# Optimization experiments

Measured on AMD Instinct MI355X. Metric: run time of the kernel, lower is better.

## Reference

```python
import jax, jax.numpy as jnp
import numpy as np

B, D, C = 8192, 1024, 4096  # batch, d_model, num_clusters (all active)
EPS = 1e-12  # matches F.normalize eps


def _l2_normalize(x):
    n = jnp.linalg.norm(x, axis=-1, keepdims=True)
    return x / jnp.maximum(n, EPS)


def setup_inputs() -> dict:
    key = jax.random.key(0)
    k1, k2 = jax.random.split(key)
    embedding = jax.random.normal(k1, (B, D), dtype=jnp.float32)
    centroids = jax.random.normal(k2, (C, D), dtype=jnp.float32)  # buffer, all active
    return {"embedding": embedding, "centroids": centroids}


def reference(embedding, centroids):
    # Fused equivalent of the per-centroid Python loop:
    # cosine sim of normalized embedding vs each normalized centroid.
    emb_n = _l2_normalize(embedding)        # [B, D]
    cen_n = _l2_normalize(centroids)        # [C, D]
    sims = jnp.clip(emb_n @ cen_n.T, 0.0, 1.0)  # [B, C], per-sim clamp to [0,1]
    max_sim = jnp.max(sims, axis=-1)        # [B]
    closest = jnp.argmax(sims, axis=-1)     # [B] int
    novelty = jnp.clip(jnp.sqrt(1.0 - max_sim), 0.0, 1.0)  # [B]
    return novelty, closest
```

## Files before the change

### kernel.cpp

```cpp
#include <hip/hip_runtime.h>
#include <math.h>

#define B_ROWS 8192
#define C_COLS 4096
#define D_DIM  1024
#define EPSN   1e-12f

typedef float v4f __attribute__((ext_vector_type(4)));
typedef short v8s __attribute__((ext_vector_type(8)));

__device__ __forceinline__ unsigned short bf16_rtn(float x) {
    unsigned int u = __float_as_uint(x);
    u += 0x7fffu + ((u >> 16) & 1u);
    return (unsigned short)(u >> 16);
}

__device__ __forceinline__ bool better_vi(float v, int i, float V, int I) {
    return (v > V) || (v == V && i < I);
}

__global__ __launch_bounds__(256) void prep_kernel(
    const float* __restrict__ emb, const float* __restrict__ cen,
    unsigned short* __restrict__ Ah, unsigned short* __restrict__ Bh,
    float* __restrict__ inv_a, float* __restrict__ inv_b)
{
    const int lane = threadIdx.x & 63;
    const int wid  = blockIdx.x * 4 + (threadIdx.x >> 6);
    const float* src; unsigned short* dst; float* invp; int r;
    if (wid < B_ROWS) { src = emb; r = wid;          dst = Ah; invp = inv_a; }
    else              { src = cen; r = wid - B_ROWS; dst = Bh; invp = inv_b; }

    const float* rp = src + (size_t)r * D_DIM;
    float4 v[4];
    float ss = 0.0f;
    #pragma unroll
    for (int j = 0; j < 4; ++j) {
        v[j] = *(const float4*)(rp + (j * 64 + lane) * 4);
        ss += v[j].x * v[j].x + v[j].y * v[j].y + v[j].z * v[j].z + v[j].w * v[j].w;
    }
    #pragma unroll
    for (int off = 1; off < 64; off <<= 1) ss += __shfl_xor(ss, off, 64);

    const float iv = 1.0f / fmaxf(sqrtf(ss), EPSN);
    if (lane == 0) invp[r] = iv;

    unsigned short* dp = dst + (size_t)r * D_DIM;
    #pragma unroll
    for (int j = 0; j < 4; ++j) {
        ushort4 H;
        H.x = bf16_rtn(v[j].x * iv);
        H.y = bf16_rtn(v[j].y * iv);
        H.z = bf16_rtn(v[j].z * iv);
        H.w = bf16_rtn(v[j].w * iv);
        *(ushort4*)(dp + (j * 64 + lane) * 4) = H;
    }
}

#define GLD16(gp, lp) \
    __builtin_amdgcn_global_load_lds( \
        (const __attribute__((address_space(1))) void*)(gp), \
        (__attribute__((address_space(3))) void*)(lp), 16, 0, 0)

__global__ __launch_bounds__(512, 4) void simmax_kernel(
    const unsigned short* __restrict__ Ahg, const unsigned short* __restrict__ Bhg,
    float* __restrict__ p1v, int* __restrict__ p1i,
    float* __restrict__ p2v, int* __restrict__ p2i)
{
    __shared__ unsigned short lds[24576];

    const int tid    = threadIdx.x;
    const int L      = tid & 63;
    const int w      = tid >> 6;
    const int lane15 = L & 15;
    const int quad   = L >> 4;
    const int wr     = w >> 1;
    const int wc     = w & 1;

    const int bid = blockIdx.x;
    const int xc  = bid & 7;
    const int s   = bid >> 3;
    const int bx  = xc * 4 + (s & 3);
    const int by  = s >> 2;
    const int row0 = bx * 256;
    const int c0   = by * 128;

    const int scol = (tid & 7) ^ ((tid >> 3) & 7);
    const unsigned short* aB = Ahg + (size_t)(row0 + (tid >> 3)) * D_DIM + scol * 8;
    const unsigned short* bB = Bhg + (size_t)(c0   + (tid >> 3)) * D_DIM + scol * 8;
    const int wofs = w * 512;

#define STAGE_ALL(kb) do { \
    GLD16(aB + (kb),           &lds[0     + wofs]); \
    GLD16(aB + 65536  + (kb),  &lds[4096  + wofs]); \
    GLD16(aB + 131072 + (kb),  &lds[8192  + wofs]); \
    GLD16(aB + 196608 + (kb),  &lds[12288 + wofs]); \
    GLD16(bB + (kb),           &lds[16384 + wofs]); \
    GLD16(bB + 65536  + (kb),  &lds[20480 + wofs]); \
} while (0)

    v4f acc[4][4];
    #pragma unroll
    for (int mt = 0; mt < 4; ++mt)
        #pragma unroll
        for (int nt = 0; nt < 4; ++nt) acc[mt][nt] = (v4f)0.0f;

    int rAo[4], rBo[4];
    #pragma unroll
    for (int t = 0; t < 4; ++t) {
        rAo[t] = (wr * 64 + t * 16 + lane15) * 64;
        rBo[t] = 16384 + (wc * 64 + t * 16 + lane15) * 64;
    }
    const int s7 = lane15 & 7;
    const int cq[2] = { (quad ^ s7) * 8, ((4 + quad) ^ s7) * 8 };

    for (int kc = 0; kc < D_DIM / 64; ++kc) {
        STAGE_ALL(kc * 64);
        __syncthreads();

        #pragma unroll
        for (int h = 0; h < 2; ++h) {
            v8s fah[4], fbh[4];
            #pragma unroll
            for (int t = 0; t < 4; ++t) {
                fah[t] = *(const v8s*)&lds[rAo[t] + cq[h]];
                fbh[t] = *(const v8s*)&lds[rBo[t] + cq[h]];
            }
            #pragma unroll
            for (int mt = 0; mt < 4; ++mt)
                #pragma unroll
                for (int nt = 0; nt < 4; ++nt)
                    acc[mt][nt] = __builtin_amdgcn_mfma_f32_16x16x32_bf16(
                        fah[mt], fbh[nt], acc[mt][nt], 0, 0, 0);
        }
        __syncthreads();
    }

    const int pc = by * 2 + wc;
    #pragma unroll
    for (int mt = 0; mt < 4; ++mt) {
        #pragma unroll
        for (int r = 0; r < 4; ++r) {
            float a1v = acc[mt][0][r];
            int   a1i = c0 + wc * 64 + 0 * 16 + lane15;
            float a2v = -1e30f;
            int   a2i = 0x7fffffff;
            #pragma unroll
            for (int nt = 1; nt < 4; ++nt) {
                float v  = acc[mt][nt][r];
                int   ci = c0 + wc * 64 + nt * 16 + lane15;
                if (better_vi(v, ci, a1v, a1i))      { a2v = a1v; a2i = a1i; a1v = v; a1i = ci; }
                else if (better_vi(v, ci, a2v, a2i)) { a2v = v;   a2i = ci; }
            }
            #pragma unroll
            for (int off = 8; off; off >>= 1) {
                float b1v = __shfl_down(a1v, off, 64); int b1i = __shfl_down(a1i, off, 64);
                float b2v = __shfl_down(a2v, off, 64); int b2i = __shfl_down(a2i, off, 64);
                if (better_vi(b1v, b1i, a1v, a1i)) {
                    if (better_vi(a1v, a1i, b2v, b2i)) { a2v = a1v; a2i = a1i; }
                    else                               { a2v = b2v; a2i = b2i; }
                    a1v = b1v; a1i = b1i;
                } else if (better_vi(b1v, b1i, a2v, a2i)) {
                    a2v = b1v; a2i = b1i;
                }
            }
            if (lane15 == 0) {
                int rg = row0 + wr * 64 + mt * 16 + quad * 4 + r;
                size_t ix = (size_t)rg * 64 + pc;
                p1v[ix] = a1v; p1i[ix] = a1i;
                p2v[ix] = a2v; p2i[ix] = a2i;
            }
        }
    }
}

__global__ __launch_bounds__(256) void finalize_kernel(
    const float* __restrict__ emb, const float* __restrict__ cen,
    const float* __restrict__ inv_a, const float* __restrict__ inv_b,
    const float* __restrict__ p1v, const int* __restrict__ p1i,
    const float* __restrict__ p2v, const int* __restrict__ p2i,
    float* __restrict__ out)
{
    const int lane = threadIdx.x & 63;
    const int row  = blockIdx.x * 4 + (threadIdx.x >> 6);
    const size_t base = (size_t)row * 64 + lane;

    float v[4]; int ix[4];
    v[0] = p1v[base]; ix[0] = p1i[base];
    v[1] = p2v[base]; ix[1] = p2i[base];
    v[2] = -1e30f;    ix[2] = 0x7ffffffe;
    v[3] = -1e30f;    ix[3] = 0x7fffffff;

    #pragma unroll
    for (int off = 1; off < 64; off <<= 1) {
        float ov[4]; int oi[4];
        #pragma unroll
        for (int k = 0; k < 4; ++k) {
            ov[k] = __shfl_xor(v[k],  off, 64);
            oi[k] = __shfl_xor(ix[k], off, 64);
        }
        #pragma unroll
        for (int k = 0; k < 4; ++k) {
            float bv = ov[k]; int bi = oi[k];
            bool b0 = better_vi(bv, bi, v[0], ix[0]);
            bool b1 = better_vi(bv, bi, v[1], ix[1]);
            bool b2 = better_vi(bv, bi, v[2], ix[2]);
            bool b3 = better_vi(bv, bi, v[3], ix[3]);
            float nv3 = b2 ? v[2] : (b3 ? bv : v[3]); int ni3 = b2 ? ix[2] : (b3 ? bi : ix[3]);
            float nv2 = b1 ? v[1] : (b2 ? bv : v[2]); int ni2 = b1 ? ix[1] : (b2 ? bi : ix[2]);
            float nv1 = b0 ? v[0] : (b1 ? bv : v[1]); int ni1 = b0 ? ix[0] : (b1 ? bi : ix[1]);
            float nv0 = b0 ? bv   : v[0];             int ni0 = b0 ? bi    : ix[0];
            v[0] = nv0; ix[0] = ni0; v[1] = nv1; ix[1] = ni1;
            v[2] = nv2; ix[2] = ni2; v[3] = nv3; ix[3] = ni3;
        }
    }

    const float* er = emb + (size_t)row * D_DIM;
    const float* cr0 = cen + (size_t)ix[0] * D_DIM;
    const float* cr1 = cen + (size_t)ix[1] * D_DIM;
    const float* cr2 = cen + (size_t)ix[2] * D_DIM;
    const float* cr3 = cen + (size_t)ix[3] * D_DIM;

    float d[4] = { 0.0f, 0.0f, 0.0f, 0.0f };
    #pragma unroll
    for (int j = 0; j < 4; ++j) {
        int e = (j * 64 + lane) * 4;
        float4 ev = *(const float4*)(er  + e);
        float4 c0 = *(const float4*)(cr0 + e);
        float4 c1 = *(const float4*)(cr1 + e);
        float4 c2 = *(const float4*)(cr2 + e);
        float4 c3 = *(const float4*)(cr3 + e);
        d[0] += ev.x * c0.x + ev.y * c0.y + ev.z * c0.z + ev.w * c0.w;
        d[1] += ev.x * c1.x + ev.y * c1.y + ev.z * c1.z + ev.w * c1.w;
        d[2] += ev.x * c2.x + ev.y * c2.y + ev.z * c2.z + ev.w * c2.w;
        d[3] += ev.x * c3.x + ev.y * c3.y + ev.z * c3.z + ev.w * c3.w;
    }
    #pragma unroll
    for (int off = 1; off < 64; off <<= 1) {
        #pragma unroll
        for (int c = 0; c < 4; ++c) d[c] += __shfl_xor(d[c], off, 64);
    }

    if (lane == 0) {
        const float ia = inv_a[row];
        float m = -1e30f; int ci = 0x7fffffff;
        #pragma unroll
        for (int c = 0; c < 4; ++c) {
            float s = d[c] * ia * inv_b[ix[c]];
            if (better_vi(s, ix[c], m, ci)) { m = s; ci = ix[c]; }
        }
        if (m <= 0.0f) ci = 0;
        float ms = fminf(fmaxf(m, 0.0f), 1.0f);
        out[row]          = fminf(fmaxf(sqrtf(1.0f - ms), 0.0f), 1.0f);
        out[B_ROWS + row] = (float)ci;
    }
}

extern "C" void kernel_launch(void* const* d_in, const int* in_sizes, int n_in,
                              void* d_out, int out_size, void* d_ws, size_t ws_size,
                              hipStream_t stream)
{
    const float* emb = (const float*)d_in[0];
    const float* cen = (const float*)d_in[1];
    float* out = (float*)d_out;

    unsigned short* Ahp = (unsigned short*)d_ws;
    unsigned short* Bhp = Ahp + (size_t)B_ROWS * D_DIM;
    float* inv_a = (float*)(Bhp + (size_t)C_COLS * D_DIM);
    float* inv_b = inv_a + B_ROWS;
    float* p1v   = inv_b + C_COLS;
    int*   p1i   = (int*)(p1v + (size_t)64 * B_ROWS);
    float* p2v   = (float*)(p1i + (size_t)64 * B_ROWS);
    int*   p2i   = (int*)(p2v + (size_t)64 * B_ROWS);

    prep_kernel<<<(B_ROWS + C_COLS) / 4, 256, 0, stream>>>(emb, cen, Ahp, Bhp, inv_a, inv_b);

    simmax_kernel<<<dim3(1024), 512, 0, stream>>>(Ahp, Bhp, p1v, p1i, p2v, p2i);

    finalize_kernel<<<B_ROWS / 4, 256, 0, stream>>>(emb, cen, inv_a, inv_b,
                                                    p1v, p1i, p2v, p2i, out);
}
```

Baseline: 201.9 us.

## Fuse finalize into simmax via last-block-per-row-band atomic counter

Drops the separate finalize kernel. Each simmax block bumps a per-row-band atomic counter after writing its partial top-2 results, and the last block of the 32 in that band does the top-4 merge, the fp32 rescoring and the output writes for its 256 rows. This removes one kernel launch and lets the finalize work overlap with GEMM blocks still running. In exchange, the tail work is serialized onto one 512-thread block per band, 32 rows per wave, which may lengthen the critical path at the end of the kernel.

```diff
diff --git a/kernel.cpp b/kernel.cpp
--- a/kernel.cpp
+++ b/kernel.cpp
@@ -22,8 +22,11 @@
 __global__ __launch_bounds__(256) void prep_kernel(
     const float* __restrict__ emb, const float* __restrict__ cen,
     unsigned short* __restrict__ Ah, unsigned short* __restrict__ Bh,
-    float* __restrict__ inv_a, float* __restrict__ inv_b)
+    float* __restrict__ inv_a, float* __restrict__ inv_b,
+    int* __restrict__ band_ctr)
 {
+    if (blockIdx.x == 0 && threadIdx.x < 32) band_ctr[threadIdx.x] = 0;
+
     const int lane = threadIdx.x & 63;
     const int wid  = blockIdx.x * 4 + (threadIdx.x >> 6);
     const float* src; unsigned short* dst; float* invp; int r;
@@ -63,10 +66,14 @@
 
 __global__ __launch_bounds__(512, 4) void simmax_kernel(
     const unsigned short* __restrict__ Ahg, const unsigned short* __restrict__ Bhg,
+    const float* __restrict__ emb, const float* __restrict__ cen,
+    const float* __restrict__ inv_a, const float* __restrict__ inv_b,
     float* __restrict__ p1v, int* __restrict__ p1i,
-    float* __restrict__ p2v, int* __restrict__ p2i)
+    float* __restrict__ p2v, int* __restrict__ p2i,
+    float* __restrict__ out, int* __restrict__ band_ctr)
 {
     __shared__ unsigned short lds[24576];
+    __shared__ int last_flag;
 
     const int tid    = threadIdx.x;
     const int L      = tid & 63;
@@ -171,87 +178,90 @@
             }
         }
     }
-}
-
-__global__ __launch_bounds__(256) void finalize_kernel(
-    const float* __restrict__ emb, const float* __restrict__ cen,
-    const float* __restrict__ inv_a, const float* __restrict__ inv_b,
-    const float* __restrict__ p1v, const int* __restrict__ p1i,
-    const float* __restrict__ p2v, const int* __restrict__ p2i,
-    float* __restrict__ out)
-{
-    const int lane = threadIdx.x & 63;
-    const int row  = blockIdx.x * 4 + (threadIdx.x >> 6);
-    const size_t base = (size_t)row * 64 + lane;
-
-    float v[4]; int ix[4];
-    v[0] = p1v[base]; ix[0] = p1i[base];
-    v[1] = p2v[base]; ix[1] = p2i[base];
-    v[2] = -1e30f;    ix[2] = 0x7ffffffe;
-    v[3] = -1e30f;    ix[3] = 0x7fffffff;
-
-    #pragma unroll
-    for (int off = 1; off < 64; off <<= 1) {
-        float ov[4]; int oi[4];
-        #pragma unroll
-        for (int k = 0; k < 4; ++k) {
-            ov[k] = __shfl_xor(v[k],  off, 64);
-            oi[k] = __shfl_xor(ix[k], off, 64);
-        }
-        #pragma unroll
-        for (int k = 0; k < 4; ++k) {
-            float bv = ov[k]; int bi = oi[k];
-            bool b0 = better_vi(bv, bi, v[0], ix[0]);
-            bool b1 = better_vi(bv, bi, v[1], ix[1]);
-            bool b2 = better_vi(bv, bi, v[2], ix[2]);
-            bool b3 = better_vi(bv, bi, v[3], ix[3]);
-            float nv3 = b2 ? v[2] : (b3 ? bv : v[3]); int ni3 = b2 ? ix[2] : (b3 ? bi : ix[3]);
-            float nv2 = b1 ? v[1] : (b2 ? bv : v[2]); int ni2 = b1 ? ix[1] : (b2 ? bi : ix[2]);
-            float nv1 = b0 ? v[0] : (b1 ? bv : v[1]); int ni1 = b0 ? ix[0] : (b1 ? bi : ix[1]);
-            float nv0 = b0 ? bv   : v[0];             int ni0 = b0 ? bi    : ix[0];
-            v[0] = nv0; ix[0] = ni0; v[1] = nv1; ix[1] = ni1;
-            v[2] = nv2; ix[2] = ni2; v[3] = nv3; ix[3] = ni3;
-        }
-    }
-
-    const float* er = emb + (size_t)row * D_DIM;
-    const float* cr0 = cen + (size_t)ix[0] * D_DIM;
-    const float* cr1 = cen + (size_t)ix[1] * D_DIM;
-    const float* cr2 = cen + (size_t)ix[2] * D_DIM;
-    const float* cr3 = cen + (size_t)ix[3] * D_DIM;
-
-    float d[4] = { 0.0f, 0.0f, 0.0f, 0.0f };
-    #pragma unroll
-    for (int j = 0; j < 4; ++j) {
-        int e = (j * 64 + lane) * 4;
-        float4 ev = *(const float4*)(er  + e);
-        float4 c0 = *(const float4*)(cr0 + e);
-        float4 c1 = *(const float4*)(cr1 + e);
-        float4 c2 = *(const float4*)(cr2 + e);
-        float4 c3 = *(const float4*)(cr3 + e);
-        d[0] += ev.x * c0.x + ev.y * c0.y + ev.z * c0.z + ev.w * c0.w;
-        d[1] += ev.x * c1.x + ev.y * c1.y + ev.z * c1.z + ev.w * c1.w;
-        d[2] += ev.x * c2.x + ev.y * c2.y + ev.z * c2.z + ev.w * c2.w;
-        d[3] += ev.x * c3.x + ev.y * c3.y + ev.z * c3.z + ev.w * c3.w;
-    }
-    #pragma unroll
-    for (int off = 1; off < 64; off <<= 1) {
-        #pragma unroll
-        for (int c = 0; c < 4; ++c) d[c] += __shfl_xor(d[c], off, 64);
-    }
-
-    if (lane == 0) {
-        const float ia = inv_a[row];
-        float m = -1e30f; int ci = 0x7fffffff;
-        #pragma unroll
-        for (int c = 0; c < 4; ++c) {
-            float s = d[c] * ia * inv_b[ix[c]];
-            if (better_vi(s, ix[c], m, ci)) { m = s; ci = ix[c]; }
-        }
-        if (m <= 0.0f) ci = 0;
-        float ms = fminf(fmaxf(m, 0.0f), 1.0f);
-        out[row]          = fminf(fmaxf(sqrtf(1.0f - ms), 0.0f), 1.0f);
-        out[B_ROWS + row] = (float)ci;
+
+    __threadfence();
+    __syncthreads();
+    if (tid == 0) {
+        int old = atomicAdd(band_ctr + bx, 1);
+        last_flag = (old == 31);
+    }
+    __syncthreads();
+    if (!last_flag) return;
+    __threadfence();
+
+    for (int rr = 0; rr < 32; ++rr) {
+        const int row = row0 + w * 32 + rr;
+        const size_t base = (size_t)row * 64 + L;
+
+        float v[4]; int ix[4];
+        v[0] = p1v[base]; ix[0] = p1i[base];
+        v[1] = p2v[base]; ix[1] = p2i[base];
+        v[2] = -1e30f;    ix[2] = 0x7ffffffe;
+        v[3] = -1e30f;    ix[3] = 0x7fffffff;
+
+        #pragma unroll
+        for (int off = 1; off < 64; off <<= 1) {
+            float ov[4]; int oi[4];
+            #pragma unroll
+            for (int k = 0; k < 4; ++k) {
+                ov[k] = __shfl_xor(v[k],  off, 64);
+                oi[k] = __shfl_xor(ix[k], off, 64);
+            }
+            #pragma unroll
+            for (int k = 0; k < 4; ++k) {
+                float bv = ov[k]; int bi = oi[k];
+                bool b0 = better_vi(bv, bi, v[0], ix[0]);
+                bool b1 = better_vi(bv, bi, v[1], ix[1]);
+                bool b2 = better_vi(bv, bi, v[2], ix[2]);
+                bool b3 = better_vi(bv, bi, v[3], ix[3]);
+                float nv3 = b2 ? v[2] : (b3 ? bv : v[3]); int ni3 = b2 ? ix[2] : (b3 ? bi : ix[3]);
+                float nv2 = b1 ? v[1] : (b2 ? bv : v[2]); int ni2 = b1 ? ix[1] : (b2 ? bi : ix[2]);
+                float nv1 = b0 ? v[0] : (b1 ? bv : v[1]); int ni1 = b0 ? ix[0] : (b1 ? bi : ix[1]);
+                float nv0 = b0 ? bv   : v[0];             int ni0 = b0 ? bi    : ix[0];
+                v[0] = nv0; ix[0] = ni0; v[1] = nv1; ix[1] = ni1;
+                v[2] = nv2; ix[2] = ni2; v[3] = nv3; ix[3] = ni3;
+            }
+        }
+
+        const float* er  = emb + (size_t)row * D_DIM;
+        const float* cr0 = cen + (size_t)ix[0] * D_DIM;
+        const float* cr1 = cen + (size_t)ix[1] * D_DIM;
+        const float* cr2 = cen + (size_t)ix[2] * D_DIM;
+        const float* cr3 = cen + (size_t)ix[3] * D_DIM;
+
+        float d[4] = { 0.0f, 0.0f, 0.0f, 0.0f };
+        #pragma unroll
+        for (int j = 0; j < 4; ++j) {
+            int e = (j * 64 + L) * 4;
+            float4 ev = *(const float4*)(er  + e);
+            float4 c0 = *(const float4*)(cr0 + e);
+            float4 c1 = *(const float4*)(cr1 + e);
+            float4 c2 = *(const float4*)(cr2 + e);
+            float4 c3 = *(const float4*)(cr3 + e);
+            d[0] += ev.x * c0.x + ev.y * c0.y + ev.z * c0.z + ev.w * c0.w;
+            d[1] += ev.x * c1.x + ev.y * c1.y + ev.z * c1.z + ev.w * c1.w;
+            d[2] += ev.x * c2.x + ev.y * c2.y + ev.z * c2.z + ev.w * c2.w;
+            d[3] += ev.x * c3.x + ev.y * c3.y + ev.z * c3.z + ev.w * c3.w;
+        }
+        #pragma unroll
+        for (int off = 1; off < 64; off <<= 1) {
+            #pragma unroll
+            for (int c = 0; c < 4; ++c) d[c] += __shfl_xor(d[c], off, 64);
+        }
+
+        if (L == 0) {
+            const float ia = inv_a[row];
+            float m = -1e30f; int ci = 0x7fffffff;
+            #pragma unroll
+            for (int c = 0; c < 4; ++c) {
+                float sc = d[c] * ia * inv_b[ix[c]];
+                if (better_vi(sc, ix[c], m, ci)) { m = sc; ci = ix[c]; }
+            }
+            if (m <= 0.0f) ci = 0;
+            float ms = fminf(fmaxf(m, 0.0f), 1.0f);
+            out[row]          = fminf(fmaxf(sqrtf(1.0f - ms), 0.0f), 1.0f);
+            out[B_ROWS + row] = (float)ci;
+        }
     }
 }
 
@@ -271,11 +281,11 @@
     int*   p1i   = (int*)(p1v + (size_t)64 * B_ROWS);
     float* p2v   = (float*)(p1i + (size_t)64 * B_ROWS);
     int*   p2i   = (int*)(p2v + (size_t)64 * B_ROWS);
-
-    prep_kernel<<<(B_ROWS + C_COLS) / 4, 256, 0, stream>>>(emb, cen, Ahp, Bhp, inv_a, inv_b);
-
-    simmax_kernel<<<dim3(1024), 512, 0, stream>>>(Ahp, Bhp, p1v, p1i, p2v, p2i);
-
-    finalize_kernel<<<B_ROWS / 4, 256, 0, stream>>>(emb, cen, inv_a, inv_b,
-                                                    p1v, p1i, p2v, p2i, out);
-}
+    int*   band_ctr = p2i + (size_t)64 * B_ROWS;
+
+    prep_kernel<<<(B_ROWS + C_COLS) / 4, 256, 0, stream>>>(
+        emb, cen, Ahp, Bhp, inv_a, inv_b, band_ctr);
+
+    simmax_kernel<<<dim3(1024), 512, 0, stream>>>(
+        Ahp, Bhp, emb, cen, inv_a, inv_b, p1v, p1i, p2v, p2i, out, band_ctr);
+}
```

After: 597.9 us. 196% more time.

## Double-buffer the A tile in LDS and prefetch the next K-chunk

Applied to the files above, without the earlier changes.

Splits the LDS staging into separate A and B loads and gives A two LDS buffers. The next A chunk is prefetched during the current chunk's MFMA work, using an explicit vmcnt wait and raw s_barrier in place of __syncthreads. The aim is to hide global-to-LDS latency for the larger A tile. In exchange, LDS per block grows from 48KB to 80KB, which can cut resident blocks per CU, and B stays single-buffered and exposed.

```diff
diff --git a/kernel.cpp b/kernel.cpp
--- a/kernel.cpp
+++ b/kernel.cpp
@@ -66,7 +66,7 @@
     float* __restrict__ p1v, int* __restrict__ p1i,
     float* __restrict__ p2v, int* __restrict__ p2i)
 {
-    __shared__ unsigned short lds[24576];
+    __shared__ unsigned short lds[40960];
 
     const int tid    = threadIdx.x;
     const int L      = tid & 63;
@@ -89,13 +89,15 @@
     const unsigned short* bB = Bhg + (size_t)(c0   + (tid >> 3)) * D_DIM + scol * 8;
     const int wofs = w * 512;
 
-#define STAGE_ALL(kb) do { \
-    GLD16(aB + (kb),           &lds[0     + wofs]); \
-    GLD16(aB + 65536  + (kb),  &lds[4096  + wofs]); \
-    GLD16(aB + 131072 + (kb),  &lds[8192  + wofs]); \
-    GLD16(aB + 196608 + (kb),  &lds[12288 + wofs]); \
-    GLD16(bB + (kb),           &lds[16384 + wofs]); \
-    GLD16(bB + 65536  + (kb),  &lds[20480 + wofs]); \
+#define STAGE_A(ab, kb) do { \
+    GLD16(aB + (kb),           &lds[(ab) + 0     + wofs]); \
+    GLD16(aB + 65536  + (kb),  &lds[(ab) + 4096  + wofs]); \
+    GLD16(aB + 131072 + (kb),  &lds[(ab) + 8192  + wofs]); \
+    GLD16(aB + 196608 + (kb),  &lds[(ab) + 12288 + wofs]); \
+} while (0)
+#define STAGE_B(kb) do { \
+    GLD16(bB + (kb),           &lds[32768 + wofs]); \
+    GLD16(bB + 65536  + (kb),  &lds[36864 + wofs]); \
 } while (0)
 
     v4f acc[4][4];
@@ -108,21 +110,32 @@
     #pragma unroll
     for (int t = 0; t < 4; ++t) {
         rAo[t] = (wr * 64 + t * 16 + lane15) * 64;
-        rBo[t] = 16384 + (wc * 64 + t * 16 + lane15) * 64;
+        rBo[t] = 32768 + (wc * 64 + t * 16 + lane15) * 64;
     }
     const int s7 = lane15 & 7;
     const int cq[2] = { (quad ^ s7) * 8, ((4 + quad) ^ s7) * 8 };
 
-    for (int kc = 0; kc < D_DIM / 64; ++kc) {
-        STAGE_ALL(kc * 64);
-        __syncthreads();
+    STAGE_A(0, 0);
+
+    int abase = 0;
+    for (int kc = 0; kc < 16; ++kc) {
+        const int kb = kc * 64;
+        STAGE_B(kb);
+        if (kc < 15) {
+            STAGE_A(abase ^ 16384, kb + 64);
+            asm volatile("s_waitcnt vmcnt(4)" ::: "memory");
+        } else {
+            asm volatile("s_waitcnt vmcnt(0)" ::: "memory");
+        }
+        __builtin_amdgcn_s_barrier();
+        __builtin_amdgcn_sched_barrier(0);
 
         #pragma unroll
         for (int h = 0; h < 2; ++h) {
             v8s fah[4], fbh[4];
             #pragma unroll
             for (int t = 0; t < 4; ++t) {
-                fah[t] = *(const v8s*)&lds[rAo[t] + cq[h]];
+                fah[t] = *(const v8s*)&lds[abase + rAo[t] + cq[h]];
                 fbh[t] = *(const v8s*)&lds[rBo[t] + cq[h]];
             }
             #pragma unroll
@@ -132,7 +145,8 @@
                     acc[mt][nt] = __builtin_amdgcn_mfma_f32_16x16x32_bf16(
                         fah[mt], fbh[nt], acc[mt][nt], 0, 0, 0);
         }
-        __syncthreads();
+        __builtin_amdgcn_s_barrier();
+        abase ^= 16384;
     }
 
     const int pc = by * 2 + wc;
```

Result: no change. 205.4 us (+1.7%).
